# Optimization experiments

Measured on AMD Instinct MI355X. Metric: run time of the kernel, lower is better.

Reference implementation:

```python
import jax, jax.numpy as jnp
import numpy as np
from jax import lax

C = 64
K = 3
RED = 8


def _lrelu(x):
    return jax.nn.leaky_relu(x, 0.1)


def setup_inputs() -> dict:
    key = jax.random.key(0)
    ks = jax.random.split(key, 8)
    b, h, w = 32, 128, 128
    x0 = jax.random.normal(ks[0], (b, C, h, w), dtype=jnp.float32)
    v = jax.random.normal(ks[1], (b, C), dtype=jnp.float32)
    s = 0.05
    # CA layer: two 1x1 convs (no bias) acting on the [b,64] embedding
    ca_w1 = jax.random.normal(ks[2], (C // RED, C), dtype=jnp.float32) * s
    ca_w2 = jax.random.normal(ks[3], (C, C // RED), dtype=jnp.float32) * s
    # kernel-generating MLP: Linear(64,64) -> LeakyReLU -> Linear(64, 64*K*K), no bias
    k_w1 = jax.random.normal(ks[4], (C, C), dtype=jnp.float32) * s
    k_w2 = jax.random.normal(ks[5], (C * K * K, C), dtype=jnp.float32) * s
    # final 1x1 conv (default_conv, bias=True)
    conv_w = jax.random.normal(ks[6], (C, C), dtype=jnp.float32) * s
    conv_b = jax.random.normal(ks[7], (C,), dtype=jnp.float32) * s
    return {"x0": x0, "v": v, "ca_w1": ca_w1, "ca_w2": ca_w2,
            "k_w1": k_w1, "k_w2": k_w2, "conv_w": conv_w, "conv_b": conv_b}


def reference(x0, v, ca_w1, ca_w2, k_w1, k_w2, conv_w, conv_b):
    b, c, h, w = x0.shape
    # Channel attention: sigmoid(W2 @ lrelu(W1 @ v)) gates x0 per (b,c)
    att = jax.nn.sigmoid(_lrelu(v @ ca_w1.T) @ ca_w2.T)  # [b, c]
    out = x0 * att[:, :, None, None]
    # Per-sample, per-channel K x K kernels generated from the embedding
    kern = (_lrelu(v @ k_w1.T) @ k_w2.T).reshape(b * c, 1, K, K)
    p = (K - 1) // 2
    y = lax.conv_general_dilated(
        out.reshape(1, b * c, h, w), kern,
        window_strides=(1, 1), padding=[(p, p), (p, p)],
        feature_group_count=b * c,
        dimension_numbers=("NCHW", "OIHW", "NCHW"))
    y = _lrelu(y).reshape(b, c, h, w)
    # final 1x1 conv with bias
    return jnp.einsum("bchw,oc->bohw", y, conv_w) + conv_b[None, :, None, None]
```

## Files before the change

kernel.cpp:

```cpp
#include <hip/hip_runtime.h>

#define HW 128
#define XBb 16
#define XBf 4
#define KTb 65552
#define LDS_BYTES 71696

typedef __attribute__((ext_vector_type(8))) short  bfrag;
typedef __attribute__((ext_vector_type(16))) float f16x;
typedef __attribute__((ext_vector_type(4)))  float f4;

__device__ __forceinline__ float lrelu(float x) { return x > 0.f ? x : 0.1f * x; }

__device__ __forceinline__ short f2bf(float f) {
    unsigned u = __builtin_bit_cast(unsigned, f);
    u = u + 0x7FFFu + ((u >> 16) & 1u);
    return (short)(u >> 16);
}
__device__ __forceinline__ float bf2f(short s) {
    return __builtin_bit_cast(float, (unsigned)(unsigned short)s << 16);
}

__device__ float g_ktab[32 * 768];
__device__ short g_whi[4096], g_wlo[4096];

__global__ __launch_bounds__(64) void dgfem_prep(
    const float* __restrict__ v, const float* __restrict__ ca_w1,
    const float* __restrict__ ca_w2, const float* __restrict__ k_w1,
    const float* __restrict__ k_w2, const float* __restrict__ conv_w)
{
    const int b = blockIdx.x;
    const int t = threadIdx.x;

    if (b == 32) {
        for (int i = t; i < 4096; i += 64) {
            float wv = conv_w[i];
            short hi = f2bf(wv);
            short lo = f2bf(wv - bf2f(hi));
            g_whi[i] = hi;
            g_wlo[i] = lo;
        }
        return;
    }

    __shared__ float vb[64], t1[8], att[64], t2[64];
    vb[t] = v[b * 64 + t];
    __syncthreads();

    if (t < 8) {
        float s = 0.f;
        for (int j = 0; j < 64; ++j) s += vb[j] * ca_w1[t * 64 + j];
        t1[t] = lrelu(s);
    }
    {
        float s = 0.f;
        for (int j = 0; j < 64; ++j) s += vb[j] * k_w1[t * 64 + j];
        t2[t] = lrelu(s);
    }
    __syncthreads();
    {
        float s = 0.f;
        for (int i = 0; i < 8; ++i) s += t1[i] * ca_w2[t * 8 + i];
        att[t] = 1.f / (1.f + expf(-s));
    }
    __syncthreads();
    for (int r = t; r < 576; r += 64) {
        int c = r / 9, tp = r - c * 9;
        float s = 0.f;
        for (int j = 0; j < 64; ++j) s += t2[j] * k_w2[r * 64 + j];
        int rr = c >> 4, gg = (c >> 3) & 1, jj = c & 7;
        g_ktab[b * 768 + ((rr * 2 + gg) * 8 + jj) * 12 + tp] = s * att[c];
    }
}

__global__ __launch_bounds__(512) void dgfem_main(
    const float* __restrict__ x0, const float* __restrict__ conv_b,
    float* __restrict__ out)
{
    const int t  = threadIdx.x;
    const int w  = t >> 6;
    const int l  = t & 63;
    const int g  = l >> 5;
    const int ln = l & 31;
    const int G  = w >> 2;
    const int wv = w & 3;
    const int px = wv * 32 + ln;

    const int bid  = blockIdx.x;
    const int orig = (bid & 7) * 256 + (bid >> 3);
    const int b    = orig >> 6;
    const int p    = orig & 63;
    const int gy0  = p * 2;
    const int gy   = gy0 + G;

    __shared__ __align__(16) char lds[LDS_BYTES];
    float* ldsf = (float*)lds;

    {
        const float* ksrc = g_ktab + b * 768;
        const float m0 = (gy0 > 0)       ? 1.f : 0.f;
        const float m1 = (gy0 + 1 < 127) ? 1.f : 0.f;
        for (int i = t; i < 768; i += 512) {
            int tp = i % 12;
            float val = (tp < 9) ? ksrc[i] : 0.f;
            float f0 = (tp < 3) ? m0 : 1.f;
            float f1 = (tp >= 6 && tp < 9) ? m1 : 1.f;
            *(float*)(lds + KTb + i * 4)        = val * f0;
            *(float*)(lds + KTb + 3072 + i * 4) = val * f1;
        }
    }

    const int l16 = l * 16;
    int soff[2];
    #pragma unroll
    for (int q = 0; q < 2; ++q) {
        int row  = gy0 - 1 + q * 2 + (l16 >> 9);
        int crow = min(max(row, 0), 127);
        soff[q]  = crow * 512 + (l16 & 511);
    }

    const char* xb = (const char*)x0 + ((size_t)b << 22);

    #define STAGE(rr_, sel_)                                                   \
    {                                                                          \
        _Pragma("unroll")                                                      \
        for (int u = 0; u < 4; ++u) {                                          \
            const int cc = 2 * w + (u >> 1);                                   \
            const int q  = u & 1;                                              \
            const char* src = xb + ((size_t)((rr_) * 16 + cc) << 16) + soff[q];\
            char* dst = lds + XBb + (sel_) * 32768 + cc * 2048 + q * 1024;     \
            __builtin_amdgcn_global_load_lds(                                  \
                (const __attribute__((address_space(1))) unsigned*)src,        \
                (__attribute__((address_space(3))) unsigned*)dst, 16, 0, 0);   \
        }                                                                      \
    }

    f16x acc0, acc1;
    #pragma unroll
    for (int i = 0; i < 16; ++i) { acc0[i] = 0.f; acc1[i] = 0.f; }

    const int   woffb = ln * 128 + g * 16;
    const float mLf = (px > 0)   ? 1.f : 0.f;
    const float mRf = (px < 127) ? 1.f : 0.f;

    STAGE(0, 0);
    __syncthreads();

    #pragma unroll 1
    for (int rr = 0; rr < 4; ++rr) {
        const int sel = rr & 1;
        if (rr < 3) STAGE(rr + 1, sel ^ 1);

        const float* xbase = ldsf + (XBf + sel * 8192 + g * 4096 + G * 128 + px - 1);
        const char*  kb = lds + KTb + G * 3072 + (rr * 2 + g) * 384;

        bfrag yh, yl;
        #pragma unroll
        for (int j = 0; j < 8; ++j) {
            const f4* kf = (const f4*)(kb + j * 48);
            f4 kA = kf[0], kB = kf[1], kC = kf[2];
            const float* bA = xbase + j * 512;
            const float* bC = bA + 256;
            float xL0 = bA[0]   * mLf;
            float xC0 = bA[1];
            float xR0 = bA[2]   * mRf;
            float xL1 = bA[128] * mLf;
            float xC1 = bA[129];
            float xR1 = bA[130] * mRf;
            float xL2 = bC[0]   * mLf;
            float xC2 = bC[1];
            float xR2 = bC[2]   * mRf;
            float a = fmaf(kA.x, xL0, fmaf(kA.y, xC0, kA.z * xR0))
                    + fmaf(kA.w, xL1, fmaf(kB.x, xC1, kB.y * xR1))
                    + fmaf(kB.z, xL2, fmaf(kB.w, xC2, kC.x * xR2));
            a = lrelu(a);
            unsigned u  = __builtin_bit_cast(unsigned, a);
            float   hif = __builtin_bit_cast(float, u & 0xFFFF0000u);
            float   lof = a - hif;
            yh[j] = (short)(u >> 16);
            yl[j] = (short)(__builtin_bit_cast(unsigned, lof) >> 16);
        }

        const char* whb = (const char*)g_whi + woffb + rr * 32;
        const char* wlb = (const char*)g_wlo + woffb + rr * 32;
        bfrag whi0 = *(const bfrag*)(whb);
        bfrag whi1 = *(const bfrag*)(whb + 4096);
        bfrag wlo0 = *(const bfrag*)(wlb);
        bfrag wlo1 = *(const bfrag*)(wlb + 4096);

        acc0 = __builtin_amdgcn_mfma_f32_32x32x16_bf16(whi0, yh, acc0, 0, 0, 0);
        acc0 = __builtin_amdgcn_mfma_f32_32x32x16_bf16(whi0, yl, acc0, 0, 0, 0);
        acc0 = __builtin_amdgcn_mfma_f32_32x32x16_bf16(wlo0, yh, acc0, 0, 0, 0);
        acc1 = __builtin_amdgcn_mfma_f32_32x32x16_bf16(whi1, yh, acc1, 0, 0, 0);
        acc1 = __builtin_amdgcn_mfma_f32_32x32x16_bf16(whi1, yl, acc1, 0, 0, 0);
        acc1 = __builtin_amdgcn_mfma_f32_32x32x16_bf16(wlo1, yh, acc1, 0, 0, 0);

        __syncthreads();
    }
    #undef STAGE

    float* ob = out + ((size_t)b << 20) + (size_t)gy * HW + px;
    #pragma unroll
    for (int q = 0; q < 4; ++q) {
        const int obase = 8 * q + 4 * g;
        float4 bv0 = *(const float4*)&conv_b[obase];
        float4 bv1 = *(const float4*)&conv_b[32 + obase];
        const float* b0f = (const float*)&bv0;
        const float* b1f = (const float*)&bv1;
        #pragma unroll
        for (int r2 = 0; r2 < 4; ++r2) {
            ob[(size_t)(obase + r2) * 16384]      = acc0[q * 4 + r2] + b0f[r2];
            ob[(size_t)(32 + obase + r2) * 16384] = acc1[q * 4 + r2] + b1f[r2];
        }
    }
}

extern "C" void kernel_launch(void* const* d_in, const int* in_sizes, int n_in,
                              void* d_out, int out_size, void* d_ws, size_t ws_size,
                              hipStream_t stream) {
    const float* x0     = (const float*)d_in[0];
    const float* v      = (const float*)d_in[1];
    const float* ca_w1  = (const float*)d_in[2];
    const float* ca_w2  = (const float*)d_in[3];
    const float* k_w1   = (const float*)d_in[4];
    const float* k_w2   = (const float*)d_in[5];
    const float* conv_w = (const float*)d_in[6];
    const float* conv_b = (const float*)d_in[7];
    float* outp = (float*)d_out;

    dgfem_prep<<<dim3(33), dim3(64), 0, stream>>>(v, ca_w1, ca_w2, k_w1, k_w2, conv_w);
    dgfem_main<<<dim3(2048), dim3(512), 0, stream>>>(x0, conv_b, outp);
}
```

Measured before the change: 84.81 us.

## Halve LDS staging per round with eight-stage channel pipeline for higher occupancy

Splits the channel staging into eight smaller rounds of 8 channels each, halving the x0 double buffer in LDS (from ~70KB to ~38KB). The kernel table is reordered to match, and the rounds are fully unrolled, with MFMAs issued every second round once a full 16-channel bf16 fragment is assembled. __launch_bounds__(512,8) is added so two 512-thread blocks can fit per CU and hide global-load latency. The cost is twice as many barriers and a heavier register-allocation constraint.

Result: slower. 279.6 us (+229.6%).

```diff
diff --git a/kernel.cpp b/kernel.cpp
--- a/kernel.cpp
+++ b/kernel.cpp
@@ -3,8 +3,8 @@
 #define HW 128
 #define XBb 16
 #define XBf 4
-#define KTb 65552
-#define LDS_BYTES 71696
+#define KTb 32784
+#define LDS_BYTES 38928
 
 typedef __attribute__((ext_vector_type(8))) short  bfrag;
 typedef __attribute__((ext_vector_type(16))) float f16x;
@@ -68,12 +68,12 @@
         int c = r / 9, tp = r - c * 9;
         float s = 0.f;
         for (int j = 0; j < 64; ++j) s += t2[j] * k_w2[r * 64 + j];
-        int rr = c >> 4, gg = (c >> 3) & 1, jj = c & 7;
-        g_ktab[b * 768 + ((rr * 2 + gg) * 8 + jj) * 12 + tp] = s * att[c];
-    }
-}
-
-__global__ __launch_bounds__(512) void dgfem_main(
+        int m = c >> 4, g = (c >> 3) & 1, a = (c >> 2) & 1, j2 = c & 3;
+        g_ktab[b * 768 + (((m * 2 + a) * 2 + g) * 4 + j2) * 12 + tp] = s * att[c];
+    }
+}
+
+__global__ __launch_bounds__(512, 8) void dgfem_main(
     const float* __restrict__ x0, const float* __restrict__ conv_b,
     float* __restrict__ out)
 {
@@ -110,29 +110,34 @@
         }
     }
 
-    const int l16 = l * 16;
-    int soff[2];
-    #pragma unroll
-    for (int q = 0; q < 2; ++q) {
-        int row  = gy0 - 1 + q * 2 + (l16 >> 9);
-        int crow = min(max(row, 0), 127);
-        soff[q]  = crow * 512 + (l16 & 511);
+    int inv0, inv1;
+    {
+        #pragma unroll
+        for (int q = 0; q < 2; ++q) {
+            int f      = q * 8192 + t * 16;
+            int slot   = f >> 11;
+            int within = f & 2047;
+            int rowq   = gy0 - 1 + (within >> 9);
+            int crow   = min(max(rowq, 0), 127);
+            int gs = slot >> 2, j2s = slot & 3;
+            int ivq = (gs * 8 + j2s) * 65536 + crow * 512 + (within & 511);
+            if (q == 0) inv0 = ivq; else inv1 = ivq;
+        }
     }
 
     const char* xb = (const char*)x0 + ((size_t)b << 22);
 
     #define STAGE(rr_, sel_)                                                   \
     {                                                                          \
-        _Pragma("unroll")                                                      \
-        for (int u = 0; u < 4; ++u) {                                          \
-            const int cc = 2 * w + (u >> 1);                                   \
-            const int q  = u & 1;                                              \
-            const char* src = xb + ((size_t)((rr_) * 16 + cc) << 16) + soff[q];\
-            char* dst = lds + XBb + (sel_) * 32768 + cc * 2048 + q * 1024;     \
-            __builtin_amdgcn_global_load_lds(                                  \
-                (const __attribute__((address_space(1))) unsigned*)src,        \
-                (__attribute__((address_space(3))) unsigned*)dst, 16, 0, 0);   \
-        }                                                                      \
+        const char* srcb = xb + ((size_t)(((rr_) >> 1) * 16 + ((rr_) & 1) * 4) << 16); \
+        __builtin_amdgcn_global_load_lds(                                      \
+            (const __attribute__((address_space(1))) unsigned*)(srcb + inv0),  \
+            (__attribute__((address_space(3))) unsigned*)(lds + XBb + (sel_) * 16384 \
+                + w * 1024), 16, 0, 0);                                        \
+        __builtin_amdgcn_global_load_lds(                                      \
+            (const __attribute__((address_space(1))) unsigned*)(srcb + inv1),  \
+            (__attribute__((address_space(3))) unsigned*)(lds + XBb + (sel_) * 16384 \
+                + 8192 + w * 1024), 16, 0, 0);                                 \
     }
 
     f16x acc0, acc1;
@@ -143,60 +148,62 @@
     const float mLf = (px > 0)   ? 1.f : 0.f;
     const float mRf = (px < 127) ? 1.f : 0.f;
 
+    bfrag yh, yl;
+
     STAGE(0, 0);
     __syncthreads();
 
-    #pragma unroll 1
-    for (int rr = 0; rr < 4; ++rr) {
-        const int sel = rr & 1;
-        if (rr < 3) STAGE(rr + 1, sel ^ 1);
-
-        const float* xbase = ldsf + (XBf + sel * 8192 + g * 4096 + G * 128 + px - 1);
-        const char*  kb = lds + KTb + G * 3072 + (rr * 2 + g) * 384;
-
-        bfrag yh, yl;
-        #pragma unroll
-        for (int j = 0; j < 8; ++j) {
-            const f4* kf = (const f4*)(kb + j * 48);
-            f4 kA = kf[0], kB = kf[1], kC = kf[2];
-            const float* bA = xbase + j * 512;
-            const float* bC = bA + 256;
-            float xL0 = bA[0]   * mLf;
-            float xC0 = bA[1];
-            float xR0 = bA[2]   * mRf;
-            float xL1 = bA[128] * mLf;
-            float xC1 = bA[129];
-            float xR1 = bA[130] * mRf;
-            float xL2 = bC[0]   * mLf;
-            float xC2 = bC[1];
-            float xR2 = bC[2]   * mRf;
-            float a = fmaf(kA.x, xL0, fmaf(kA.y, xC0, kA.z * xR0))
-                    + fmaf(kA.w, xL1, fmaf(kB.x, xC1, kB.y * xR1))
-                    + fmaf(kB.z, xL2, fmaf(kB.w, xC2, kC.x * xR2));
-            a = lrelu(a);
-            unsigned u  = __builtin_bit_cast(unsigned, a);
-            float   hif = __builtin_bit_cast(float, u & 0xFFFF0000u);
-            float   lof = a - hif;
-            yh[j] = (short)(u >> 16);
-            yl[j] = (short)(__builtin_bit_cast(unsigned, lof) >> 16);
-        }
-
-        const char* whb = (const char*)g_whi + woffb + rr * 32;
-        const char* wlb = (const char*)g_wlo + woffb + rr * 32;
-        bfrag whi0 = *(const bfrag*)(whb);
-        bfrag whi1 = *(const bfrag*)(whb + 4096);
-        bfrag wlo0 = *(const bfrag*)(wlb);
-        bfrag wlo1 = *(const bfrag*)(wlb + 4096);
-
-        acc0 = __builtin_amdgcn_mfma_f32_32x32x16_bf16(whi0, yh, acc0, 0, 0, 0);
-        acc0 = __builtin_amdgcn_mfma_f32_32x32x16_bf16(whi0, yl, acc0, 0, 0, 0);
-        acc0 = __builtin_amdgcn_mfma_f32_32x32x16_bf16(wlo0, yh, acc0, 0, 0, 0);
-        acc1 = __builtin_amdgcn_mfma_f32_32x32x16_bf16(whi1, yh, acc1, 0, 0, 0);
-        acc1 = __builtin_amdgcn_mfma_f32_32x32x16_bf16(whi1, yl, acc1, 0, 0, 0);
-        acc1 = __builtin_amdgcn_mfma_f32_32x32x16_bf16(wlo1, yh, acc1, 0, 0, 0);
-
-        __syncthreads();
-    }
+    #define ROUND(rr_, a_, m_, sel_)                                           \
+    {                                                                          \
+        if ((rr_) < 7) STAGE((rr_) + 1, (sel_) ^ 1);                           \
+        const float* xbase = ldsf + (XBf + (sel_) * 4096 + g * 2048            \
+                                     + G * 128 + px - 1);                      \
+        const char*  kb = lds + KTb + G * 3072 + ((rr_) * 8 + g * 4) * 48;     \
+        _Pragma("unroll")                                                      \
+        for (int j2 = 0; j2 < 4; ++j2) {                                       \
+            const f4* kf = (const f4*)(kb + j2 * 48);                          \
+            f4 kA = kf[0], kB = kf[1], kC = kf[2];                             \
+            const float* bA = xbase + j2 * 512;                                \
+            float xL0 = bA[0]   * mLf, xC0 = bA[1],   xR0 = bA[2]   * mRf;     \
+            float xL1 = bA[128] * mLf, xC1 = bA[129], xR1 = bA[130] * mRf;     \
+            float xL2 = bA[256] * mLf, xC2 = bA[257], xR2 = bA[258] * mRf;     \
+            float aY = fmaf(kA.x, xL0, fmaf(kA.y, xC0, kA.z * xR0))            \
+                     + fmaf(kA.w, xL1, fmaf(kB.x, xC1, kB.y * xR1))            \
+                     + fmaf(kB.z, xL2, fmaf(kB.w, xC2, kC.x * xR2));           \
+            aY = lrelu(aY);                                                    \
+            unsigned uY = __builtin_bit_cast(unsigned, aY);                    \
+            float hif = __builtin_bit_cast(float, uY & 0xFFFF0000u);           \
+            yh[(a_) * 4 + j2] = (short)(uY >> 16);                             \
+            yl[(a_) * 4 + j2] =                                                \
+                (short)(__builtin_bit_cast(unsigned, aY - hif) >> 16);         \
+        }                                                                      \
+        if (a_) {                                                              \
+            const char* whb = (const char*)g_whi + woffb + (m_) * 32;          \
+            const char* wlb = (const char*)g_wlo + woffb + (m_) * 32;          \
+            bfrag whi0 = *(const bfrag*)(whb);                                 \
+            bfrag whi1 = *(const bfrag*)(whb + 4096);                          \
+            bfrag wlo0 = *(const bfrag*)(wlb);                                 \
+            bfrag wlo1 = *(const bfrag*)(wlb + 4096);                          \
+            acc0 = __builtin_amdgcn_mfma_f32_32x32x16_bf16(whi0, yh, acc0, 0, 0, 0); \
+            acc0 = __builtin_amdgcn_mfma_f32_32x32x16_bf16(whi0, yl, acc0, 0, 0, 0); \
+            acc0 = __builtin_amdgcn_mfma_f32_32x32x16_bf16(wlo0, yh, acc0, 0, 0, 0); \
+            acc1 = __builtin_amdgcn_mfma_f32_32x32x16_bf16(whi1, yh, acc1, 0, 0, 0); \
+            acc1 = __builtin_amdgcn_mfma_f32_32x32x16_bf16(whi1, yl, acc1, 0, 0, 0); \
+            acc1 = __builtin_amdgcn_mfma_f32_32x32x16_bf16(wlo1, yh, acc1, 0, 0, 0); \
+        }                                                                      \
+        if ((rr_) < 7) __syncthreads();                                        \
+    }
+
+    ROUND(0, 0, 0, 0);
+    ROUND(1, 1, 0, 1);
+    ROUND(2, 0, 1, 0);
+    ROUND(3, 1, 1, 1);
+    ROUND(4, 0, 2, 0);
+    ROUND(5, 1, 2, 1);
+    ROUND(6, 0, 3, 0);
+    ROUND(7, 1, 3, 1);
+
+    #undef ROUND
     #undef STAGE
 
     float* ob = out + ((size_t)b << 20) + (size_t)gy * HW + px;
```
